# Performance work log

Hardware: AMD Instinct MI355X
Metric: run time of the kernel (lower is better)

The kernel has to match this reference:

```python
import jax, jax.numpy as jnp
import numpy as np

N = 20000
IN_CH, HID, OUT_CH = 512, 64, 16
H1, H2 = 8, 1
NEG_SLOPE = 0.2


def setup_inputs() -> dict:
    key = jax.random.key(0)
    ks = jax.random.split(key, 10)
    E = 320000
    x = jax.random.normal(ks[0], (N, IN_CH), dtype=jnp.float32)
    edge_index = jax.random.randint(ks[1], (2, E), 0, N, dtype=jnp.int64)
    s = 0.05
    return {
        "x": x,
        "edge_index": edge_index,
        "W1": jax.random.normal(ks[2], (H1 * HID, IN_CH), dtype=jnp.float32) * s,
        "att_src1": jax.random.normal(ks[3], (1, H1, HID), dtype=jnp.float32) * s,
        "att_dst1": jax.random.normal(ks[4], (1, H1, HID), dtype=jnp.float32) * s,
        "b1": jnp.zeros((H1 * HID,), dtype=jnp.float32),
        "W2": jax.random.normal(ks[5], (H2 * OUT_CH, H1 * HID), dtype=jnp.float32) * s,
        "att_src2": jax.random.normal(ks[6], (1, H2, OUT_CH), dtype=jnp.float32) * s,
        "att_dst2": jax.random.normal(ks[7], (1, H2, OUT_CH), dtype=jnp.float32) * s,
        "b2": jnp.zeros((OUT_CH,), dtype=jnp.float32),
    }


def _gat_conv(x, src, dst, W, att_src, att_dst, bias, heads, out_ch, concat):
    # Linear transform: [N, H, C]
    h = (x @ W.T).reshape(x.shape[0], heads, out_ch)
    n = x.shape[0]
    # Per-node attention logits (a_src . h), (a_dst . h): [N, H]
    a_s = (h * att_src).sum(-1)
    a_d = (h * att_dst).sum(-1)
    # Edge-wise LeakyReLU attention: [E, H]
    e = a_s[src] + a_d[dst]
    e = jnp.where(e >= 0, e, NEG_SLOPE * e)
    # Segment softmax over incoming edges of each destination node
    m = jax.ops.segment_max(e, dst, num_segments=n)
    p = jnp.exp(e - m[dst])
    z = jax.ops.segment_sum(p, dst, num_segments=n)
    alpha = p / z[dst]  # [E, H]
    # Weighted scatter-aggregate: out[dst] += alpha * h[src]
    msg = h[src] * alpha[:, :, None]  # [E, H, C]
    out = jax.ops.segment_sum(msg, dst, num_segments=n)
    out = out.reshape(n, heads * out_ch) if concat else out.mean(axis=1)
    return out + bias


def reference(x, edge_index, W1, att_src1, att_dst1, b1, W2, att_src2, att_dst2, b2):
    # PyG GATConv adds self-loops by default
    loops = jnp.arange(N, dtype=edge_index.dtype)
    src = jnp.concatenate([edge_index[0], loops])
    dst = jnp.concatenate([edge_index[1], loops])
    # dropout layers are identity in eval mode
    h = _gat_conv(x, src, dst, W1, att_src1, att_dst1, b1, H1, HID, True)
    h = jax.nn.relu(h)
    out = _gat_conv(h, src, dst, W2, att_src2, att_dst2, b2, H2, OUT_CH, False)
    return out
```

## Files before the change

kernel.cpp:

```cpp
#include <hip/hip_runtime.h>

#define Nn     20000
#define IN_CH  512
#define C1     512
#define H1n    8
#define HIDn   64
#define OUT_CH 16
#define En     320000
#define EPn    340000
#define NEG    0.2f

typedef __attribute__((ext_vector_type(8))) short bf16x8;
typedef __attribute__((ext_vector_type(4))) float f32x4;

__device__ inline unsigned short bf16_rne(float f) {
  unsigned int u = __float_as_uint(f);
  return (unsigned short)((u + 0x7fffu + ((u >> 16) & 1u)) >> 16);
}
__device__ inline float bf16_f(unsigned short u) {
  return __uint_as_float(((unsigned int)u) << 16);
}

__device__ inline bf16x8 pack8(float4 f0, float4 f1) {
  unsigned int r0, r1, r2, r3;
  asm("v_cvt_pk_bf16_f32 %0, %1, %2" : "=v"(r0) : "v"(f0.x), "v"(f0.y));
  asm("v_cvt_pk_bf16_f32 %0, %1, %2" : "=v"(r1) : "v"(f0.z), "v"(f0.w));
  asm("v_cvt_pk_bf16_f32 %0, %1, %2" : "=v"(r2) : "v"(f1.x), "v"(f1.y));
  asm("v_cvt_pk_bf16_f32 %0, %1, %2" : "=v"(r3) : "v"(f1.z), "v"(f1.w));
  union { unsigned int u[4]; bf16x8 v; } un;
  un.u[0] = r0; un.u[1] = r1; un.u[2] = r2; un.u[3] = r3;
  return un.v;
}

#define NW8  (C1 * IN_CH / 8)
#define NW28 (OUT_CH * C1 / 8)
#define NH4  (EPn / 4)
__global__ __launch_bounds__(256) void cvtwh_kernel(
    const float* __restrict__ W1, unsigned short* __restrict__ w1b,
    const float* __restrict__ W2, unsigned short* __restrict__ w2b,
    const int* __restrict__ ei, int* __restrict__ cnt)
{
  int i = blockIdx.x * 256 + threadIdx.x;
  const float* in; unsigned short* ob; int idx;
  if (i < NW8) { in = W1; ob = w1b; idx = i; }
  else if (i < NW8 + NW28) { in = W2; ob = w2b; idx = i - NW8; }
  else if (i < NW8 + NW28 + NH4) {
    int e4 = (i - NW8 - NW28) * 4;
    if (e4 < En) {
      int4 dv = *(const int4*)&ei[En + e4];
      atomicAdd(&cnt[dv.x], 1); atomicAdd(&cnt[dv.y], 1);
      atomicAdd(&cnt[dv.z], 1); atomicAdd(&cnt[dv.w], 1);
    } else {
      int d = e4 - En;
      atomicAdd(&cnt[d], 1);     atomicAdd(&cnt[d + 1], 1);
      atomicAdd(&cnt[d + 2], 1); atomicAdd(&cnt[d + 3], 1);
    }
    return;
  } else return;
  float4 f0 = ((const float4*)in)[idx * 2];
  float4 f1 = ((const float4*)in)[idx * 2 + 1];
  float f[8] = {f0.x, f0.y, f0.z, f0.w, f1.x, f1.y, f1.z, f1.w};
  unsigned short h[8];
#pragma unroll
  for (int j = 0; j < 8; j++) h[j] = bf16_rne(f[j]);
  ushort4 hv0 = {h[0], h[1], h[2], h[3]}, hv1 = {h[4], h[5], h[6], h[7]};
  ((ushort4*)ob)[idx * 2] = hv0; ((ushort4*)ob)[idx * 2 + 1] = hv1;
}

#define GLL(gp, lp) __builtin_amdgcn_global_load_lds( \
    (const __attribute__((address_space(1))) void*)(gp), \
    (__attribute__((address_space(3))) void*)(lp), 16, 0, 0)

#define SWZ(c)  ((c) ^ (((c) >> 3) & 3))
#define SWZA(c) ((c) ^ (((c) >> 3) & 7))

__global__ __launch_bounds__(256, 3) void gemm1_mfma(
    const float* __restrict__ Af, const unsigned short* __restrict__ Bb,
    const float* __restrict__ attS, const float* __restrict__ attD,
    unsigned short* __restrict__ Cb, float* __restrict__ as1, float* __restrict__ ad1)
{
  __shared__ float sAf[128 * 32];
  __shared__ unsigned short sB[128 * 32];
  int t = threadIdx.x;
  int wgid = blockIdx.x;
  int bm = (wgid & 7) + 8 * (wgid >> 5);
  int bn = (wgid >> 3) & 3;
  if (bm >= 157) return;
  int lane = t & 63, w = t >> 6;

  int acb[4]; size_t aoff[4];
#pragma unroll
  for (int q = 0; q < 4; q++) {
    int slot = w * 256 + q * 64 + lane;
    acb[q] = w * 256 + q * 64;
    int cs = SWZA(slot);
    int ra = bm * 128 + (cs >> 3); if (ra > Nn - 1) ra = Nn - 1;
    aoff[q] = (size_t)ra * IN_CH + (cs & 7) * 4;
  }
  int slot0 = w * 128 + lane, slot1 = slot0 + 64;
  int bcb0 = w * 128, bcb1 = w * 128 + 64;
  int cs0 = SWZ(slot0), cs1 = SWZ(slot1);
  int br0 = bn * 128 + (cs0 >> 2);
  int br1 = bn * 128 + (cs1 >> 2);
  size_t offB0 = (size_t)br0 * IN_CH + (cs0 & 3) * 8;
  size_t offB1 = (size_t)br1 * IN_CH + (cs1 & 3) * 8;

  int wm = (w >> 1) * 64, wn = (w & 1) * 64;
  int lr = lane & 15, kb = lane >> 4;

  f32x4 acc[4][4] = {};

  for (int k0 = 0; k0 < IN_CH; k0 += 32) {
    __syncthreads();
    GLL(Af + aoff[0] + k0, sAf + acb[0] * 4);
    GLL(Af + aoff[1] + k0, sAf + acb[1] * 4);
    GLL(Af + aoff[2] + k0, sAf + acb[2] * 4);
    GLL(Af + aoff[3] + k0, sAf + acb[3] * 4);
    GLL(Bb + offB0 + k0, sB + bcb0 * 8);
    GLL(Bb + offB1 + k0, sB + bcb1 * 8);
    __syncthreads();

    bf16x8 ah[4], bh[4];
#pragma unroll
    for (int i = 0; i < 4; i++) {
      int c0 = (wm + i * 16 + lr) * 8 + kb * 2;
      float4 f0 = *(const float4*)&sAf[SWZA(c0) * 4];
      float4 f1 = *(const float4*)&sAf[SWZA(c0 + 1) * 4];
      ah[i] = pack8(f0, f1);
      int rcb = (wn + i * 16 + lr) * 4 + kb;
      bh[i] = *(const bf16x8*)&sB[SWZ(rcb) * 8];
    }
#pragma unroll
    for (int i = 0; i < 4; i++)
#pragma unroll
      for (int j = 0; j < 4; j++)
        acc[i][j] = __builtin_amdgcn_mfma_f32_16x16x32_bf16(ah[i], bh[j], acc[i][j], 0, 0, 0);
  }

  int lq = lane >> 4;
#pragma unroll
  for (int i = 0; i < 4; i++) {
    int r0 = bm * 128 + wm + i * 16 + lq * 4;
#pragma unroll
    for (int j = 0; j < 4; j++) {
      int ccol = bn * 128 + wn + j * 16 + lr;
#pragma unroll
      for (int q = 0; q < 4; q++) {
        unsigned int myv = bf16_rne(acc[i][j][q]);
        unsigned int pv = __shfl_xor(myv, 1);
        int r = r0 + q;
        if (!(lr & 1) && r < Nn) {
          unsigned int word = myv | (pv << 16);
          *(unsigned int*)&Cb[(size_t)r * C1 + ccol] = word;
        }
      }
    }
  }
  int hh = bn * 2 + (wn >> 6);
  float aSj[4], aDj[4];
#pragma unroll
  for (int j = 0; j < 4; j++) {
    int cc = bn * 128 + wn + j * 16 + lr;
    aSj[j] = attS[cc]; aDj[j] = attD[cc];
  }
#pragma unroll
  for (int i = 0; i < 4; i++)
#pragma unroll
    for (int q = 0; q < 4; q++) {
      float s = acc[i][0][q] * aSj[0] + acc[i][1][q] * aSj[1]
              + acc[i][2][q] * aSj[2] + acc[i][3][q] * aSj[3];
      float dd = acc[i][0][q] * aDj[0] + acc[i][1][q] * aDj[1]
               + acc[i][2][q] * aDj[2] + acc[i][3][q] * aDj[3];
#pragma unroll
      for (int off = 1; off < 16; off <<= 1) {
        s += __shfl_xor(s, off);
        dd += __shfl_xor(dd, off);
      }
      int r = bm * 128 + wm + i * 16 + lq * 4 + q;
      if (lr == 0 && r < Nn) { as1[r * 8 + hh] = s; ad1[r * 8 + hh] = dd; }
    }
}

__global__ __launch_bounds__(1024) void scan_kernel(
    const int* __restrict__ cnt, int* __restrict__ row)
{
  extern __shared__ int sm[];
  __shared__ int wsum[16];
  int t = threadIdx.x;

  for (int i = t; i < Nn; i += 1024) {
    int c = i / 20, o = i - c * 20;
    sm[c * 21 + o] = cnt[i];
  }
  __syncthreads();

  int v[20];
  int s = 0;
  if (t < 1000) {
    int base = t * 21;
#pragma unroll
    for (int j = 0; j < 20; j++) {
      int c = sm[base + j];
      v[j] = s;
      s += c;
    }
  }
  int lane = t & 63, w = t >> 6;
  int incl = s;
#pragma unroll
  for (int off = 1; off < 64; off <<= 1) {
    int o = __shfl_up(incl, off);
    if (lane >= off) incl += o;
  }
  if (lane == 63) wsum[w] = incl;
  __syncthreads();
  if (w == 0) {
    int ws = (lane < 16) ? wsum[lane] : 0;
#pragma unroll
    for (int off = 1; off < 16; off <<= 1) {
      int o = __shfl_up(ws, off);
      if (lane >= off) ws += o;
    }
    if (lane < 16) wsum[lane] = ws;
  }
  __syncthreads();
  int excl = ((w > 0) ? wsum[w - 1] : 0) + incl - s;
  if (t < 1000) {
    int base = t * 21;
#pragma unroll
    for (int j = 0; j < 20; j++) sm[base + j] = excl + v[j];
  }
  __syncthreads();
  for (int i = t; i < Nn; i += 1024) {
    int c = i / 20, o = i - c * 20;
    row[i] = sm[c * 21 + o];
  }
  if (t == 0) row[Nn] = EPn;
}

__global__ void scatter_kernel(const int* __restrict__ ei, const int* __restrict__ row,
                               int* __restrict__ cur, int* __restrict__ csr)
{
  int e4 = (blockIdx.x * 256 + threadIdx.x) * 4;
  if (e4 >= EPn) return;
  if (e4 < En) {
    int4 sv = *(const int4*)&ei[e4];
    int4 dv = *(const int4*)&ei[En + e4];
    int sa[4] = {sv.x, sv.y, sv.z, sv.w};
    int da[4] = {dv.x, dv.y, dv.z, dv.w};
#pragma unroll
    for (int j = 0; j < 4; j++) {
      int pos = row[da[j]] + atomicAdd(&cur[da[j]], 1);
      csr[pos] = sa[j];
    }
  } else {
#pragma unroll
    for (int j = 0; j < 4; j++) {
      int d = e4 - En + j;
      int pos = row[d] + atomicAdd(&cur[d], 1);
      csr[pos] = d;
    }
  }
}

__global__ __launch_bounds__(256, 6) void agg1_kernel(
    const int* __restrict__ row, const int* __restrict__ csr,
    const unsigned short* __restrict__ h1b, const float* __restrict__ as1,
    const float* __restrict__ adv, const float* __restrict__ b1,
    const unsigned short* __restrict__ W2b,
    const float* __restrict__ attS2, const float* __restrict__ attD2,
    float* __restrict__ h2, float* __restrict__ as2, float* __restrict__ ad2)
{
  __shared__ float part[2][64 * 9];

  int t = threadIdx.x, lane = t & 63, w = t >> 6;
  int pr = w >> 1;
  int p  = w & 1;
  int d = blockIdx.x * 2 + pr;
  int beg = row[d], end = row[d + 1];
  int deg = end - beg;
  int hq = lane >> 3;
  size_t chb = (size_t)8 * lane;
  float adH = adv[d * 8 + hq];

  float a0 = 0.f, a1 = 0.f, a2 = 0.f, a3 = 0.f;
  float a4 = 0.f, a5 = 0.f, a6 = 0.f, a7 = 0.f;
  float z = 0.f;
  int nj = (deg - p + 1) >> 1;
#pragma unroll 4
  for (int j = 0; j < nj; j++) {
    int e = beg + p + 2 * j;
    int s = csr[e];
    float v = as1[s * 8 + hq] + adH;
    v = (v >= 0.f) ? v : NEG * v;
    float pp = __expf(v);
    z += pp;
    uint4 u = *(const uint4*)&h1b[(size_t)s * C1 + chb];
    a0 = fmaf(pp, __uint_as_float(u.x << 16), a0);
    a1 = fmaf(pp, __uint_as_float(u.x & 0xffff0000u), a1);
    a2 = fmaf(pp, __uint_as_float(u.y << 16), a2);
    a3 = fmaf(pp, __uint_as_float(u.y & 0xffff0000u), a3);
    a4 = fmaf(pp, __uint_as_float(u.z << 16), a4);
    a5 = fmaf(pp, __uint_as_float(u.z & 0xffff0000u), a5);
    a6 = fmaf(pp, __uint_as_float(u.w << 16), a6);
    a7 = fmaf(pp, __uint_as_float(u.w & 0xffff0000u), a7);
  }

  if (p == 1) {
    float* ps = &part[pr][lane * 9];
    ps[0] = a0; ps[1] = a1; ps[2] = a2; ps[3] = a3;
    ps[4] = a4; ps[5] = a5; ps[6] = a6; ps[7] = a7; ps[8] = z;
  }
  __syncthreads();
  if (p == 0) {
    const float* ps = &part[pr][lane * 9];
    a0 += ps[0]; a1 += ps[1]; a2 += ps[2]; a3 += ps[3];
    a4 += ps[4]; a5 += ps[5]; a6 += ps[6]; a7 += ps[7]; z += ps[8];
    float rz = 1.f / z;
    float4 b0 = *(const float4*)&b1[chb];
    float4 b4 = *(const float4*)&b1[chb + 4];
    float o0 = fmaf(a0, rz, b0.x); o0 = o0 > 0.f ? o0 : 0.f;
    float o1 = fmaf(a1, rz, b0.y); o1 = o1 > 0.f ? o1 : 0.f;
    float o2 = fmaf(a2, rz, b0.z); o2 = o2 > 0.f ? o2 : 0.f;
    float o3 = fmaf(a3, rz, b0.w); o3 = o3 > 0.f ? o3 : 0.f;
    float o4 = fmaf(a4, rz, b4.x); o4 = o4 > 0.f ? o4 : 0.f;
    float o5 = fmaf(a5, rz, b4.y); o5 = o5 > 0.f ? o5 : 0.f;
    float o6 = fmaf(a6, rz, b4.z); o6 = o6 > 0.f ? o6 : 0.f;
    float o7 = fmaf(a7, rz, b4.w); o7 = o7 > 0.f ? o7 : 0.f;

    float myh2 = 0.f, s2 = 0.f, d2 = 0.f;
#pragma unroll
    for (int j = 0; j < OUT_CH; j++) {
      bf16x8 wv = *(const bf16x8*)&W2b[j * 512 + chb];
      float pj = o0 * bf16_f((unsigned short)wv[0]) + o1 * bf16_f((unsigned short)wv[1])
               + o2 * bf16_f((unsigned short)wv[2]) + o3 * bf16_f((unsigned short)wv[3])
               + o4 * bf16_f((unsigned short)wv[4]) + o5 * bf16_f((unsigned short)wv[5])
               + o6 * bf16_f((unsigned short)wv[6]) + o7 * bf16_f((unsigned short)wv[7]);
#pragma unroll
      for (int off = 1; off < 64; off <<= 1) pj += __shfl_xor(pj, off);
      if (lane == j) myh2 = pj;
      s2 = fmaf(pj, attS2[j], s2);
      d2 = fmaf(pj, attD2[j], d2);
    }
    if (lane < OUT_CH) h2[(size_t)d * OUT_CH + lane] = myh2;
    if (lane == 0) { as2[d] = s2; ad2[d] = d2; }
  }
}

__global__ __launch_bounds__(256) void agg2_kernel(
    const int* __restrict__ row, const int* __restrict__ csr,
    const float* __restrict__ h2, const float* __restrict__ as2,
    const float* __restrict__ ad2, const float* __restrict__ b2,
    float* __restrict__ out)
{
  int wave = threadIdx.x >> 6, lane = threadIdx.x & 63;
  int d = blockIdx.x * 4 + wave;
  int beg = row[d], end = row[d + 1];
  float add = ad2[d];

  int c = lane & 15;
  float acc = 0.f, z = 0.f;
  for (int e = beg + (lane >> 4); e < end; e += 4) {
    int s = csr[e];
    float v = as2[s] + add;
    v = (v >= 0.f) ? v : NEG * v;
    float p = __expf(v);
    z += p;
    acc = fmaf(p, h2[(size_t)s * 16 + c], acc);
  }
  acc += __shfl_xor(acc, 16);
  acc += __shfl_xor(acc, 32);
  z += __shfl_xor(z, 16);
  z += __shfl_xor(z, 32);
  if (lane < 16) out[(size_t)d * 16 + lane] = acc / z + b2[lane];
}

extern "C" void kernel_launch(void* const* d_in, const int* in_sizes, int n_in,
                              void* d_out, int out_size, void* d_ws, size_t ws_size,
                              hipStream_t stream)
{
  const float* x    = (const float*)d_in[0];
  const int*   ei   = (const int*)d_in[1];
  const float* W1   = (const float*)d_in[2];
  const float* asv1 = (const float*)d_in[3];
  const float* adv1 = (const float*)d_in[4];
  const float* b1   = (const float*)d_in[5];
  const float* W2   = (const float*)d_in[6];
  const float* asv2 = (const float*)d_in[7];
  const float* adv2 = (const float*)d_in[8];
  const float* b2   = (const float*)d_in[9];
  float* out = (float*)d_out;

  unsigned short* h1b = (unsigned short*)d_ws;
  unsigned short* w_b = h1b + (size_t)Nn * C1;
  unsigned short* w2b = w_b + (size_t)C1 * IN_CH;
  float* as1   = (float*)(w2b + (size_t)OUT_CH * C1);
  float* ad1   = as1 + (size_t)Nn * H1n;
  float* h2    = ad1 + (size_t)Nn * H1n;
  float* as2   = h2 + (size_t)Nn * OUT_CH;
  float* ad2   = as2 + Nn;
  int* csr  = (int*)(ad2 + Nn);
  int* cnt  = csr + EPn;
  int* cur  = cnt + Nn;
  int* rowp = cur + Nn;

  hipMemsetAsync(cnt, 0, 2 * Nn * sizeof(int), stream);

  cvtwh_kernel<<<(NW8 + NW28 + NH4 + 255) / 256, 256, 0, stream>>>(
      W1, w_b, W2, w2b, ei, cnt);

  gemm1_mfma<<<640, 256, 0, stream>>>(x, w_b, asv1, adv1, h1b, as1, ad1);

  scan_kernel<<<1, 1024, 1000 * 21 * sizeof(int), stream>>>(cnt, rowp);
  scatter_kernel<<<(EPn / 4 + 255) / 256, 256, 0, stream>>>(ei, rowp, cur, csr);
  agg1_kernel<<<Nn / 2, 256, 0, stream>>>(rowp, csr, h1b, as1, ad1, b1,
                                          w2b, asv2, adv2, h2, as2, ad2);
  agg2_kernel<<<Nn / 4, 256, 0, stream>>>(rowp, csr, h2, as2, ad2, b2, out);
}
```

Measured before the change: 140.9 us.

## Double-buffer LDS tiles in gemm1 to overlap global loads with MFMA

```diff
diff --git a/kernel.cpp b/kernel.cpp
--- a/kernel.cpp
+++ b/kernel.cpp
@@ -79,8 +79,8 @@
     const float* __restrict__ attS, const float* __restrict__ attD,
     unsigned short* __restrict__ Cb, float* __restrict__ as1, float* __restrict__ ad1)
 {
-  __shared__ float sAf[128 * 32];
-  __shared__ unsigned short sB[128 * 32];
+  __shared__ float sAf[2][128 * 32];
+  __shared__ unsigned short sB[2][128 * 32];
   int t = threadIdx.x;
   int wgid = blockIdx.x;
   int bm = (wgid & 7) + 8 * (wgid >> 5);
@@ -110,31 +110,46 @@
 
   f32x4 acc[4][4] = {};
 
-  for (int k0 = 0; k0 < IN_CH; k0 += 32) {
-    __syncthreads();
-    GLL(Af + aoff[0] + k0, sAf + acb[0] * 4);
-    GLL(Af + aoff[1] + k0, sAf + acb[1] * 4);
-    GLL(Af + aoff[2] + k0, sAf + acb[2] * 4);
-    GLL(Af + aoff[3] + k0, sAf + acb[3] * 4);
-    GLL(Bb + offB0 + k0, sB + bcb0 * 8);
-    GLL(Bb + offB1 + k0, sB + bcb1 * 8);
-    __syncthreads();
-
+  GLL(Af + aoff[0], sAf[0] + acb[0] * 4);
+  GLL(Af + aoff[1], sAf[0] + acb[1] * 4);
+  GLL(Af + aoff[2], sAf[0] + acb[2] * 4);
+  GLL(Af + aoff[3], sAf[0] + acb[3] * 4);
+  GLL(Bb + offB0, sB[0] + bcb0 * 8);
+  GLL(Bb + offB1, sB[0] + bcb1 * 8);
+  __syncthreads();
+
+#pragma unroll 2
+  for (int it = 0; it < 16; it++) {
+    int cur = it & 1;
+    const float* Ac = sAf[cur];
+    const unsigned short* Bc = sB[cur];
     bf16x8 ah[4], bh[4];
 #pragma unroll
     for (int i = 0; i < 4; i++) {
       int c0 = (wm + i * 16 + lr) * 8 + kb * 2;
-      float4 f0 = *(const float4*)&sAf[SWZA(c0) * 4];
-      float4 f1 = *(const float4*)&sAf[SWZA(c0 + 1) * 4];
+      float4 f0 = *(const float4*)&Ac[SWZA(c0) * 4];
+      float4 f1 = *(const float4*)&Ac[SWZA(c0 + 1) * 4];
       ah[i] = pack8(f0, f1);
       int rcb = (wn + i * 16 + lr) * 4 + kb;
-      bh[i] = *(const bf16x8*)&sB[SWZ(rcb) * 8];
+      bh[i] = *(const bf16x8*)&Bc[SWZ(rcb) * 8];
+    }
+    if (it < 15) {
+      int k1 = (it + 1) * 32;
+      float* An = sAf[cur ^ 1];
+      unsigned short* Bn = sB[cur ^ 1];
+      GLL(Af + aoff[0] + k1, An + acb[0] * 4);
+      GLL(Af + aoff[1] + k1, An + acb[1] * 4);
+      GLL(Af + aoff[2] + k1, An + acb[2] * 4);
+      GLL(Af + aoff[3] + k1, An + acb[3] * 4);
+      GLL(Bb + offB0 + k1, Bn + bcb0 * 8);
+      GLL(Bb + offB1 + k1, Bn + bcb1 * 8);
     }
 #pragma unroll
     for (int i = 0; i < 4; i++)
 #pragma unroll
       for (int j = 0; j < 4; j++)
         acc[i][j] = __builtin_amdgcn_mfma_f32_16x16x32_bf16(ah[i], bh[j], acc[i][j], 0, 0, 0);
+    __syncthreads();
   }
 
   int lq = lane >> 4;
```

Measured after the change: 140.8 us, median of 2. No clear change (-0.1%).
